# Performance work log

Measured on AMD Instinct MI355X. Metric: run time of the kernel, lower is better.

The kernel has to match this reference:

```python
import jax, jax.numpy as jnp
from jax import lax
import numpy as np

B = 4096        # num_batch
NVAR = 120      # 3 * num_legs(4) * horizon(10)
NC = 2 * NVAR   # num_constraints = 240
HID = 1024      # GRU hidden size
RIN = 3 * (NC + NVAR)  # GRU input dim = 1080
MAXITER = 8
RHO = 1.0
REG = 1e-4


def setup_inputs() -> dict:
    key = jax.random.key(0)
    ks = jax.random.split(key, 10)
    # SPD quadratic cost H, linear cost g, inequality constraints C x <= c
    M = jax.random.normal(ks[0], (NVAR, NVAR), jnp.float32)
    H = M @ M.T / NVAR + jnp.eye(NVAR, dtype=jnp.float32)
    g = jax.random.normal(ks[1], (NVAR,), jnp.float32)
    C = 0.1 * jax.random.normal(ks[2], (NC, NVAR), jnp.float32)
    c = jax.random.uniform(ks[3], (NC,), jnp.float32, 0.1, 1.0)
    lamda_init = jax.random.normal(ks[4], (B, NVAR), jnp.float32)
    s_init = jax.random.uniform(ks[5], (B, NC), jnp.float32)
    h_0 = jnp.zeros((B, HID), jnp.float32)
    # GRU cell (torch GRUCell layout: [3*HID, in]) + output head to NC+NVAR
    sc_i = 1.0 / np.sqrt(RIN)
    sc_h = 1.0 / np.sqrt(HID)
    W_ih = sc_i * jax.random.normal(ks[6], (3 * HID, RIN), jnp.float32)
    b_ih = jnp.zeros((3 * HID,), jnp.float32)
    W_hh = sc_h * jax.random.normal(ks[7], (3 * HID, HID), jnp.float32)
    b_hh = jnp.zeros((3 * HID,), jnp.float32)
    W_out = sc_h * jax.random.normal(ks[8], (NC + NVAR, HID), jnp.float32)
    b_out = jnp.zeros((NC + NVAR,), jnp.float32)
    return dict(lamda_init=lamda_init, s_init=s_init, h_0=h_0, H=H, g=g, C=C, c=c,
                W_ih=W_ih, b_ih=b_ih, W_hh=W_hh, b_hh=b_hh, W_out=W_out, b_out=b_out)


def _gru_cell(x, h, W_ih, b_ih, W_hh, b_hh):
    gi = x @ W_ih.T + b_ih
    gh = h @ W_hh.T + b_hh
    i_r, i_z, i_n = jnp.split(gi, 3, axis=1)
    h_r, h_z, h_n = jnp.split(gh, 3, axis=1)
    r = jax.nn.sigmoid(i_r + h_r)
    z = jax.nn.sigmoid(i_z + h_z)
    n = jnp.tanh(i_n + r * h_n)
    return (1.0 - z) * n + z * h


def reference(lamda_init, s_init, h_0, H, g, C, c, W_ih, b_ih, W_hh, b_hh, W_out, b_out):
    I = jnp.eye(NVAR, dtype=H.dtype)
    # ---- init solve (compute_projection_gru preamble) ----
    Q_inv0 = jnp.linalg.pinv(H + REG * I)
    lincost0 = -0.0 * lamda_init + g                 # [B, NVAR]
    xi0 = (-lincost0) @ Q_inv0.T                     # sol = (Qinv @ rhs.T).T
    s0 = jnp.maximum(0.0, -(xi0 @ C.T) + c)
    s0 = 0.0 * s_init + s0                           # s_init = 0*nn + 1*s_
    lam0 = lamda_init
    # ---- constant per-iteration projection matrix (same every iter) ----
    Q_inv = jnp.linalg.pinv(H + RHO * (C.T @ C) + REG * I)

    def step(carry, _):
        s, lam, h = carry
        # compute_feasible_control
        b_aug = c - s                                # [B, NC]
        lincost = -lam + g - RHO * (b_aug @ C)       # [B, NVAR]
        xi = (-lincost) @ Q_inv.T                    # [B, NVAR]
        Axi = xi @ C.T                               # [B, NC]
        s_new = jnp.maximum(0.0, -Axi + c)
        res_vec = Axi - c + s_new
        res_norm = jnp.linalg.norm(res_vec, axis=1)
        lam_new = lam - RHO * (res_vec @ C)
        qp_cost = 0.5 * (xi @ H @ xi.T) + xi @ g     # [B, B] (faithful to source)
        qp_norm = jnp.linalg.norm(qp_cost, axis=1)
        # GRU refinement
        r = jnp.concatenate([s, lam, s_new, lam_new, s_new - s, lam_new - lam], axis=1)
        h_new = _gru_cell(r, h, W_ih, b_ih, W_hh, b_hh)
        out = h_new @ W_out.T + b_out                # [B, NC+NVAR]
        s_fin = jnp.maximum(0.0, s_new + out[:, :NC])
        lam_fin = lam_new + out[:, NC:NC + NVAR]
        fixed = jnp.linalg.norm(lam - lam_fin, axis=1) + jnp.linalg.norm(s - s_fin, axis=1)
        return (s_fin, lam_fin, h_new), (xi, res_norm, fixed, qp_norm)

    (_, _, _), (xis, primal, fixed, qpres) = lax.scan(step, (s0, lam0, h_0), None, length=MAXITER)
    return xis[-1], primal, fixed, qpres
```

## Files before the change

kernel.cpp:

```cpp
#include <hip/hip_runtime.h>
#include <hip/hip_bf16.h>
#include <math.h>

#define NB    4096
#define NV    120
#define NCN   240
#define HIDD  1024
#define RINN  1080
#define NOUTD 360
#define NOUTP 384
#define NITER 8
#define REGEPS 1e-4f
#define NPART 256

#define KCAT 4224
#define HOFF 2176
#define KWC  2112
#define KWO  1024
#define NSTEP_R 34
#define NSTEPS  66

typedef unsigned short u16;
typedef __attribute__((ext_vector_type(8))) short short8v;
typedef __attribute__((ext_vector_type(4))) float f32x4;

__device__ inline u16 f2b(float x) {
    __hip_bfloat16 h = __float2bfloat16(x);
    return __builtin_bit_cast(u16, h);
}
__device__ inline float b2f(u16 u) {
    __hip_bfloat16 h = __builtin_bit_cast(__hip_bfloat16, u);
    return __bfloat162float(h);
}

__device__ inline void gl16(const void* g, void* l) {
    __builtin_amdgcn_global_load_lds(
        (__attribute__((address_space(1))) void*)(void*)g,
        (__attribute__((address_space(3))) void*)l, 16, 0, 0);
}

__global__ void k_buildA(const float* __restrict__ H, const float* __restrict__ C,
                         float* __restrict__ A, float* __restrict__ A0) {
    int i = blockIdx.x;
    int which = blockIdx.y;
    for (int j = threadIdx.x; j < NV; j += blockDim.x) {
        float v = H[i*NV + j] + (i == j ? REGEPS : 0.f);
        if (which == 0) {
            float acc = 0.f;
            for (int k = 0; k < NCN; ++k) acc += C[k*NV + i] * C[k*NV + j];
            A[i*NV + j] = v + acc;
        } else {
            A0[i*NV + j] = v;
        }
    }
}

__global__ void k_buildCT(const float* __restrict__ C, float* __restrict__ CT) {
    int j = blockIdx.x;
    for (int k = threadIdx.x; k < NCN; k += 256)
        CT[(size_t)j * NCN + k] = C[(size_t)k * NV + j];
}

__device__ inline void inv4x4(const float* m, float* inv) {
    float s0 = m[0]*m[5] - m[1]*m[4];
    float s1 = m[0]*m[6] - m[2]*m[4];
    float s2 = m[0]*m[7] - m[3]*m[4];
    float s3 = m[1]*m[6] - m[2]*m[5];
    float s4 = m[1]*m[7] - m[3]*m[5];
    float s5 = m[2]*m[7] - m[3]*m[6];
    float c5 = m[10]*m[15] - m[11]*m[14];
    float c4 = m[9]*m[15] - m[11]*m[13];
    float c3 = m[9]*m[14] - m[10]*m[13];
    float c2 = m[8]*m[15] - m[11]*m[12];
    float c1 = m[8]*m[14] - m[10]*m[12];
    float c0 = m[8]*m[13] - m[9]*m[12];
    float det = s0*c5 - s1*c4 + s2*c3 + s3*c2 - s4*c1 + s5*c0;
    float id = 1.0f / det;
    inv[0]  = ( m[5]*c5 - m[6]*c4 + m[7]*c3) * id;
    inv[1]  = (-m[1]*c5 + m[2]*c4 - m[3]*c3) * id;
    inv[2]  = ( m[13]*s5 - m[14]*s4 + m[15]*s3) * id;
    inv[3]  = (-m[9]*s5 + m[10]*s4 - m[11]*s3) * id;
    inv[4]  = (-m[4]*c5 + m[6]*c2 - m[7]*c1) * id;
    inv[5]  = ( m[0]*c5 - m[2]*c2 + m[3]*c1) * id;
    inv[6]  = (-m[12]*s5 + m[14]*s2 - m[15]*s1) * id;
    inv[7]  = ( m[8]*s5 - m[10]*s2 + m[11]*s1) * id;
    inv[8]  = ( m[4]*c4 - m[5]*c2 + m[7]*c0) * id;
    inv[9]  = (-m[0]*c4 + m[1]*c2 - m[3]*c0) * id;
    inv[10] = ( m[12]*s4 - m[13]*s2 + m[15]*s0) * id;
    inv[11] = (-m[8]*s4 + m[9]*s2 - m[11]*s0) * id;
    inv[12] = (-m[4]*c3 + m[5]*c1 - m[6]*c0) * id;
    inv[13] = ( m[0]*c3 - m[1]*c1 + m[2]*c0) * id;
    inv[14] = (-m[12]*s3 + m[13]*s1 - m[14]*s0) * id;
    inv[15] = ( m[8]*s3 - m[9]*s1 + m[10]*s0) * id;
}

__global__ __launch_bounds__(1024) void k_invert(const float* __restrict__ Ain,
                                                 const float* __restrict__ A0in,
                                                 float* __restrict__ Qi,
                                                 float* __restrict__ Qi0) {
    __shared__ float M[NV][132];
    __shared__ float Rl[4][132];
    __shared__ float Bl[16];
    const float* src = (blockIdx.x == 0) ? Ain : A0in;
    float* dst = (blockIdx.x == 0) ? Qi : Qi0;
    const int t = threadIdx.x;
    for (int idx = t; idx < NV*132; idx += 1024) {
        int i = idx / 132, j = idx - i*132;
        M[i][j] = (j < NV) ? src[i*NV + j] : 0.f;
    }
    __syncthreads();
    const int ty = t >> 5;
    const int g4 = (t & 31) * 4;
    for (int kk = 0; kk < NV; kk += 4) {
        if (ty == 0) {
            float a[16], b[16];
            #pragma unroll
            for (int p = 0; p < 4; ++p) {
                float4 v = *(const float4*)&M[kk + p][kk];
                a[p*4+0] = v.x; a[p*4+1] = v.y; a[p*4+2] = v.z; a[p*4+3] = v.w;
            }
            inv4x4(a, b);
            float4 m0v = *(const float4*)&M[kk+0][g4];
            float4 m1v = *(const float4*)&M[kk+1][g4];
            float4 m2v = *(const float4*)&M[kk+2][g4];
            float4 m3v = *(const float4*)&M[kk+3][g4];
            #pragma unroll
            for (int p = 0; p < 4; ++p) {
                float4 r;
                r.x = b[p*4+0]*m0v.x + b[p*4+1]*m1v.x + b[p*4+2]*m2v.x + b[p*4+3]*m3v.x;
                r.y = b[p*4+0]*m0v.y + b[p*4+1]*m1v.y + b[p*4+2]*m2v.y + b[p*4+3]*m3v.y;
                r.z = b[p*4+0]*m0v.z + b[p*4+1]*m1v.z + b[p*4+2]*m2v.z + b[p*4+3]*m3v.z;
                r.w = b[p*4+0]*m0v.w + b[p*4+1]*m1v.w + b[p*4+2]*m2v.w + b[p*4+3]*m3v.w;
                *(float4*)&Rl[p][g4] = r;
            }
            if (t < 16) Bl[t] = b[t];
        }
        float4 F[4];
        #pragma unroll
        for (int q = 0; q < 4; ++q) {
            int i = ty + 32*q;
            F[q] = (i < NV) ? *(const float4*)&M[i][kk] : float4{0.f,0.f,0.f,0.f};
        }
        __syncthreads();
        #pragma unroll
        for (int q = 0; q < 4; ++q) {
            int i = ty + 32*q;
            if (i < NV) {
                int dp = i - kk;
                bool ispiv = (dp >= 0) && (dp < 4);
                float4 v;
                if (g4 == kk) {
                    if (ispiv) {
                        v = *(const float4*)&Bl[dp*4];
                    } else {
                        v.x = -(F[q].x*Bl[0] + F[q].y*Bl[4] + F[q].z*Bl[8]  + F[q].w*Bl[12]);
                        v.y = -(F[q].x*Bl[1] + F[q].y*Bl[5] + F[q].z*Bl[9]  + F[q].w*Bl[13]);
                        v.z = -(F[q].x*Bl[2] + F[q].y*Bl[6] + F[q].z*Bl[10] + F[q].w*Bl[14]);
                        v.w = -(F[q].x*Bl[3] + F[q].y*Bl[7] + F[q].z*Bl[11] + F[q].w*Bl[15]);
                    }
                } else if (ispiv) {
                    v = *(const float4*)&Rl[dp][g4];
                } else {
                    float4 r0 = *(const float4*)&Rl[0][g4];
                    float4 r1 = *(const float4*)&Rl[1][g4];
                    float4 r2 = *(const float4*)&Rl[2][g4];
                    float4 r3 = *(const float4*)&Rl[3][g4];
                    v = *(const float4*)&M[i][g4];
                    v.x -= F[q].x*r0.x + F[q].y*r1.x + F[q].z*r2.x + F[q].w*r3.x;
                    v.y -= F[q].x*r0.y + F[q].y*r1.y + F[q].z*r2.y + F[q].w*r3.y;
                    v.z -= F[q].x*r0.z + F[q].y*r1.z + F[q].z*r2.z + F[q].w*r3.z;
                    v.w -= F[q].x*r0.w + F[q].y*r1.w + F[q].z*r2.w + F[q].w*r3.w;
                }
                *(float4*)&M[i][g4] = v;
            }
        }
        __syncthreads();
    }
    for (int idx = t; idx < NV*NV; idx += 1024) {
        int i = idx / NV, j = idx - i*NV;
        dst[idx] = M[i][j];
    }
}

__global__ void k_s0(const float* __restrict__ Qi0, const float* __restrict__ g,
                     const float* __restrict__ C, const float* __restrict__ c,
                     float* __restrict__ s0v) {
    __shared__ float xi0[NV];
    int t = threadIdx.x;
    if (t < NV) {
        float a = 0.f;
        for (int j = 0; j < NV; ++j) a += Qi0[t*NV + j] * g[j];
        xi0[t] = -a;
    }
    __syncthreads();
    if (t < NCN) {
        float a = 0.f;
        for (int j = 0; j < NV; ++j) a += C[t*NV + j] * xi0[j];
        s0v[t] = fmaxf(0.f, c[t] - a);
    }
}

__global__ void k_init(const float* __restrict__ s0v, const float* __restrict__ lam0,
                       float* __restrict__ s, float* __restrict__ lam) {
    int b0 = blockIdx.x * 8;
    int t = threadIdx.x;
    for (int idx = t; idx < 8*NCN; idx += 256) {
        int m = idx / NCN, k = idx % NCN;
        s[(size_t)(b0 + m)*NCN + k] = s0v[k];
    }
    for (int idx = t; idx < 8*NV; idx += 256) lam[(size_t)b0*NV + idx] = lam0[(size_t)b0*NV + idx];
}

__global__ void k_packH(const float* __restrict__ h0, u16* __restrict__ act) {
    int n = blockIdx.x;
    size_t base = (size_t)n * KCAT + HOFF;
    for (int k = threadIdx.x; k < HIDD; k += 256) {
        float x = h0[(size_t)n * HIDD + k];
        u16 hi = f2b(x);
        act[base + k] = hi;
        act[base + HIDD + k] = f2b(x - b2f(hi));
    }
}

__global__ void k_packWcat(const float* __restrict__ Wih, const float* __restrict__ Whh,
                           u16* __restrict__ Wc) {
    int n = blockIdx.x;
    size_t base = (size_t)n * KWC;
    for (int k = threadIdx.x; k < 1088; k += 256)
        Wc[base + k] = f2b(k < RINN ? Wih[(size_t)n * RINN + k] : 0.f);
    for (int k = threadIdx.x; k < HIDD; k += 256)
        Wc[base + 1088 + k] = f2b(Whh[(size_t)n * HIDD + k]);
}

__global__ void k_packWo(const float* __restrict__ src, u16* __restrict__ dst) {
    int n = blockIdx.x;
    size_t row = (size_t)n * KWO;
    for (int k = threadIdx.x; k < KWO; k += 256)
        dst[row + k] = f2b(n < NOUTD ? src[(size_t)n * HIDD + k] : 0.f);
}

__device__ inline void write2(u16* __restrict__ act, size_t base, int pos, float x) {
    u16 hi = f2b(x);
    u16 lo = f2b(x - b2f(hi));
    act[base + pos] = hi;
    act[base + 1088 + pos] = lo;
}

__device__ inline float hadd4(float4 v) { return (v.x + v.y) + (v.z + v.w); }

#define XB 8
__global__ __launch_bounds__(512) void k_xiproj(
        const float* __restrict__ s, const float* __restrict__ lam,
        const float* __restrict__ Cg, const float* __restrict__ CTg,
        const float* __restrict__ c,
        const float* __restrict__ g, const float* __restrict__ Qi,
        const float* __restrict__ Hg,
        float* __restrict__ xi, float* __restrict__ Y, float* __restrict__ wv,
        float* __restrict__ snew, float* __restrict__ lamn,
        u16* __restrict__ act, float* __restrict__ primal) {
    __shared__ float Msh[31680];
    __shared__ float bd[XB][NCN];
    __shared__ float ul[XB][NV];
    __shared__ float xl[XB][NV];
    __shared__ float resl[XB][NCN];
    const int b0 = blockIdx.x * XB;
    const int t = threadIdx.x;

    for (int idx = t; idx < XB*NCN; idx += 512) {
        int m = idx / NCN, k = idx - m*NCN;
        bd[m][k] = c[k] - s[(size_t)(b0 + m)*NCN + k];
    }
    for (int idx = t; idx < NV*NCN; idx += 512) {
        int i = idx / NCN, k = idx - i*NCN;
        Msh[i*244 + k] = CTg[idx];
    }
    __syncthreads();
    if (t < 240) {
        int m = t / 30, jb = t - (t / 30) * 30;
        float4 a0 = {0,0,0,0}, a1 = {0,0,0,0}, a2 = {0,0,0,0}, a3 = {0,0,0,0};
        for (int kg = 0; kg < 60; ++kg) {
            float4 b4 = *(const float4*)&bd[m][kg*4];
            float4 c0 = *(const float4*)&Msh[(jb     ) * 244 + kg*4];
            float4 c1 = *(const float4*)&Msh[(jb + 30) * 244 + kg*4];
            float4 c2 = *(const float4*)&Msh[(jb + 60) * 244 + kg*4];
            float4 c3 = *(const float4*)&Msh[(jb + 90) * 244 + kg*4];
            a0.x += b4.x*c0.x; a0.y += b4.y*c0.y; a0.z += b4.z*c0.z; a0.w += b4.w*c0.w;
            a1.x += b4.x*c1.x; a1.y += b4.y*c1.y; a1.z += b4.z*c1.z; a1.w += b4.w*c1.w;
            a2.x += b4.x*c2.x; a2.y += b4.y*c2.y; a2.z += b4.z*c2.z; a2.w += b4.w*c2.w;
            a3.x += b4.x*c3.x; a3.y += b4.y*c3.y; a3.z += b4.z*c3.z; a3.w += b4.w*c3.w;
        }
        #pragma unroll
        for (int p = 0; p < 4; ++p) {
            int j = jb + 30*p;
            float h = (p == 0) ? hadd4(a0) : (p == 1) ? hadd4(a1) : (p == 2) ? hadd4(a2) : hadd4(a3);
            ul[m][j] = lam[(size_t)(b0 + m)*NV + j] - g[j] + h;
        }
    }
    __syncthreads();
    for (int idx = t; idx < NV*NV; idx += 512) {
        int i = idx / NV, j = idx - i*NV;
        Msh[i*132 + j] = Qi[idx];
        Msh[(120 + i)*132 + j] = Hg[idx];
    }
    __syncthreads();
    if (t < 240) {
        int m = t / 30, ib = t - (t / 30) * 30;
        float4 a0 = {0,0,0,0}, a1 = {0,0,0,0}, a2 = {0,0,0,0}, a3 = {0,0,0,0};
        for (int jg = 0; jg < 30; ++jg) {
            float4 u4 = *(const float4*)&ul[m][jg*4];
            float4 q0 = *(const float4*)&Msh[(ib     ) * 132 + jg*4];
            float4 q1 = *(const float4*)&Msh[(ib + 30) * 132 + jg*4];
            float4 q2 = *(const float4*)&Msh[(ib + 60) * 132 + jg*4];
            float4 q3 = *(const float4*)&Msh[(ib + 90) * 132 + jg*4];
            a0.x += u4.x*q0.x; a0.y += u4.y*q0.y; a0.z += u4.z*q0.z; a0.w += u4.w*q0.w;
            a1.x += u4.x*q1.x; a1.y += u4.y*q1.y; a1.z += u4.z*q1.z; a1.w += u4.w*q1.w;
            a2.x += u4.x*q2.x; a2.y += u4.y*q2.y; a2.z += u4.z*q2.z; a2.w += u4.w*q2.w;
            a3.x += u4.x*q3.x; a3.y += u4.y*q3.y; a3.z += u4.z*q3.z; a3.w += u4.w*q3.w;
        }
        #pragma unroll
        for (int p = 0; p < 4; ++p) {
            int i = ib + 30*p;
            float a = (p == 0) ? hadd4(a0) : (p == 1) ? hadd4(a1) : (p == 2) ? hadd4(a2) : hadd4(a3);
            xl[m][i] = a;
            xi[(size_t)(b0 + m)*NV + i] = a;
        }
    }
    __syncthreads();
    if (t < 240) {
        int m = t / 30, ib = t - (t / 30) * 30;
        float4 a0 = {0,0,0,0}, a1 = {0,0,0,0}, a2 = {0,0,0,0}, a3 = {0,0,0,0};
        for (int jg = 0; jg < 30; ++jg) {
            float4 x4 = *(const float4*)&xl[m][jg*4];
            float4 h0 = *(const float4*)&Msh[(120 + ib     ) * 132 + jg*4];
            float4 h1 = *(const float4*)&Msh[(120 + ib + 30) * 132 + jg*4];
            float4 h2 = *(const float4*)&Msh[(120 + ib + 60) * 132 + jg*4];
            float4 h3 = *(const float4*)&Msh[(120 + ib + 90) * 132 + jg*4];
            a0.x += x4.x*h0.x; a0.y += x4.y*h0.y; a0.z += x4.z*h0.z; a0.w += x4.w*h0.w;
            a1.x += x4.x*h1.x; a1.y += x4.y*h1.y; a1.z += x4.z*h1.z; a1.w += x4.w*h1.w;
            a2.x += x4.x*h2.x; a2.y += x4.y*h2.y; a2.z += x4.z*h2.z; a2.w += x4.w*h2.w;
            a3.x += x4.x*h3.x; a3.y += x4.y*h3.y; a3.z += x4.z*h3.z; a3.w += x4.w*h3.w;
        }
        #pragma unroll
        for (int p = 0; p < 4; ++p) {
            int i = ib + 30*p;
            float a = (p == 0) ? hadd4(a0) : (p == 1) ? hadd4(a1) : (p == 2) ? hadd4(a2) : hadd4(a3);
            Y[(size_t)(b0 + m)*NV + i] = a;
        }
    }
    if (t >= 240 && t < 240 + XB) {
        int m = t - 240;
        float a = 0.f;
        for (int j = 0; j < NV; ++j) a += xl[m][j] * g[j];
        wv[b0 + m] = a;
    }
    __syncthreads();
    for (int idx = t; idx < NCN*NV; idx += 512) {
        int k = idx / NV, j = idx - k*NV;
        Msh[k*132 + j] = Cg[idx];
    }
    __syncthreads();
    if (t < 480) {
        int m = t / 60, kb = t - (t / 60) * 60;
        float4 a0 = {0,0,0,0}, a1 = {0,0,0,0}, a2 = {0,0,0,0}, a3 = {0,0,0,0};
        for (int jg = 0; jg < 30; ++jg) {
            float4 x4 = *(const float4*)&xl[m][jg*4];
            float4 c0 = *(const float4*)&Msh[(kb      ) * 132 + jg*4];
            float4 c1 = *(const float4*)&Msh[(kb + 60 ) * 132 + jg*4];
            float4 c2 = *(const float4*)&Msh[(kb + 120) * 132 + jg*4];
            float4 c3 = *(const float4*)&Msh[(kb + 180) * 132 + jg*4];
            a0.x += x4.x*c0.x; a0.y += x4.y*c0.y; a0.z += x4.z*c0.z; a0.w += x4.w*c0.w;
            a1.x += x4.x*c1.x; a1.y += x4.y*c1.y; a1.z += x4.z*c1.z; a1.w += x4.w*c1.w;
            a2.x += x4.x*c2.x; a2.y += x4.y*c2.y; a2.z += x4.z*c2.z; a2.w += x4.w*c2.w;
            a3.x += x4.x*c3.x; a3.y += x4.y*c3.y; a3.z += x4.z*c3.z; a3.w += x4.w*c3.w;
        }
        #pragma unroll
        for (int p = 0; p < 4; ++p) {
            int k = kb + 60*p;
            float a = (p == 0) ? hadd4(a0) : (p == 1) ? hadd4(a1) : (p == 2) ? hadd4(a2) : hadd4(a3);
            float sn = fmaxf(0.f, c[k] - a);
            float rv = a - c[k] + sn;
            resl[m][k] = rv;
            int b = b0 + m;
            snew[(size_t)b*NCN + k] = sn;
            float so = s[(size_t)b*NCN + k];
            size_t base = (size_t)b * KCAT;
            write2(act, base, k, so);
            write2(act, base, 360 + k, sn);
            write2(act, base, 720 + k, sn - so);
        }
    }
    __syncthreads();
    if (t < XB) {
        float a = 0.f;
        for (int k = 0; k < NCN; ++k) a += resl[t][k] * resl[t][k];
        primal[b0 + t] = sqrtf(a);
    }
    for (int idx = t; idx < NV*NCN; idx += 512) {
        int i = idx / NCN, k = idx - i*NCN;
        Msh[i*244 + k] = CTg[idx];
    }
    __syncthreads();
    if (t < 240) {
        int m = t / 30, ib = t - (t / 30) * 30;
        float4 a0 = {0,0,0,0}, a1 = {0,0,0,0}, a2 = {0,0,0,0}, a3 = {0,0,0,0};
        for (int kg = 0; kg < 60; ++kg) {
            float4 r4 = *(const float4*)&resl[m][kg*4];
            float4 c0 = *(const float4*)&Msh[(ib     ) * 244 + kg*4];
            float4 c1 = *(const float4*)&Msh[(ib + 30) * 244 + kg*4];
            float4 c2 = *(const float4*)&Msh[(ib + 60) * 244 + kg*4];
            float4 c3 = *(const float4*)&Msh[(ib + 90) * 244 + kg*4];
            a0.x += r4.x*c0.x; a0.y += r4.y*c0.y; a0.z += r4.z*c0.z; a0.w += r4.w*c0.w;
            a1.x += r4.x*c1.x; a1.y += r4.y*c1.y; a1.z += r4.z*c1.z; a1.w += r4.w*c1.w;
            a2.x += r4.x*c2.x; a2.y += r4.y*c2.y; a2.z += r4.z*c2.z; a2.w += r4.w*c2.w;
            a3.x += r4.x*c3.x; a3.y += r4.y*c3.y; a3.z += r4.z*c3.z; a3.w += r4.w*c3.w;
        }
        #pragma unroll
        for (int p = 0; p < 4; ++p) {
            int i = ib + 30*p;
            float a = (p == 0) ? hadd4(a0) : (p == 1) ? hadd4(a1) : (p == 2) ? hadd4(a2) : hadd4(a3);
            int b = b0 + m;
            float lo = lam[(size_t)b*NV + i];
            float ln = lo - a;
            lamn[(size_t)b*NV + i] = ln;
            size_t base = (size_t)b * KCAT;
            write2(act, base, 240 + i, lo);
            write2(act, base, 600 + i, ln);
            write2(act, base, 960 + i, ln - lo);
        }
    }
    for (int idx = t; idx < XB*8; idx += 512) {
        int m = idx >> 3, k = 1080 + (idx & 7);
        size_t base = (size_t)(b0 + m) * KCAT;
        act[base + k] = 0;
        act[base + 1088 + k] = 0;
    }
}

__global__ __launch_bounds__(256) void k_qp_part(const float* __restrict__ xi, const float* __restrict__ wv,
                         double* __restrict__ Gp, double* __restrict__ vp, double* __restrict__ Sp) {
    __shared__ float xl[16][NV];
    __shared__ float wl[16];
    int p = blockIdx.x;
    int b0 = p * 16;
    int t = threadIdx.x;
    for (int idx = t; idx < 16*NV; idx += 256) xl[idx/NV][idx%NV] = xi[(size_t)b0*NV + idx];
    if (t < 16) wl[t] = wv[b0 + t];
    __syncthreads();
    for (int idx = t; idx < NV*NV; idx += 256) {
        int i = idx / NV, j = idx % NV;
        double a = 0.0;
        for (int m = 0; m < 16; ++m) a += (double)xl[m][i] * (double)xl[m][j];
        Gp[(size_t)p*NV*NV + idx] = a;
    }
    if (t < NV) {
        double a = 0.0;
        for (int m = 0; m < 16; ++m) a += (double)wl[m] * (double)xl[m][t];
        vp[(size_t)p*NV + t] = a;
    }
    if (t == 0) {
        double a = 0.0;
        for (int m = 0; m < 16; ++m) a += (double)wl[m] * (double)wl[m];
        Sp[p] = a;
    }
}

__global__ void k_qp_red(const double* __restrict__ Gp, const double* __restrict__ vp,
                         const double* __restrict__ Sp,
                         double* __restrict__ G, double* __restrict__ v, double* __restrict__ S) {
    int idx = blockIdx.x * 256 + threadIdx.x;
    if (idx < NV*NV) {
        double a = 0.0;
        for (int p = 0; p < NPART; ++p) a += Gp[(size_t)p*NV*NV + idx];
        G[idx] = a;
    }
    if (idx < NV) {
        double a = 0.0;
        for (int p = 0; p < NPART; ++p) a += vp[(size_t)p*NV + idx];
        v[idx] = a;
    }
    if (idx == 0) {
        double a = 0.0;
        for (int p = 0; p < NPART; ++p) a += Sp[p];
        S[0] = a;
    }
}

__global__ __launch_bounds__(256) void k_qp_norm(const float* __restrict__ Y, const double* __restrict__ G,
                         const double* __restrict__ v, const double* __restrict__ S,
                         float* __restrict__ qp) {
    __shared__ float Yl[16][NV];
    __shared__ double tl[16][NV];
    int b0 = blockIdx.x * 16;
    int t = threadIdx.x;
    for (int idx = t; idx < 16*NV; idx += 256) Yl[idx/NV][idx%NV] = Y[(size_t)b0*NV + idx];
    __syncthreads();
    for (int idx = t; idx < 16*NV; idx += 256) {
        int m = idx / NV, i = idx % NV;
        double a = 0.0;
        for (int j = 0; j < NV; ++j) a += G[j*NV + i] * (double)Yl[m][j];
        tl[m][i] = a;
    }
    __syncthreads();
    if (t < 16) {
        double a = 0.0, bv = 0.0;
        for (int i = 0; i < NV; ++i) { a += (double)Yl[t][i] * tl[t][i]; bv += (double)Yl[t][i] * v[i]; }
        double q = 0.25 * a + bv + S[0];
        qp[b0 + t] = (float)sqrt(q > 0.0 ? q : 0.0);
    }
}

#define GRUF_STEP(NSLOT, BUFI) do {                                              \
    char* Ah_ = lds + (BUFI) * 32768;                                            \
    char* Al_ = Ah_ + 4096;                                                      \
    char* Bb_ = Ah_ + 8192;                                                      \
    const int srow = lane & 15;                                                  \
    const int ksl = lane >> 4;                                                   \
    short8v ah[2], al[2];                                                        \
    _Pragma("unroll")                                                            \
    for (int fm = 0; fm < 2; ++fm) {                                             \
        int rr = wm * 32 + fm * 16 + srow;                                       \
        int off = rr * 64 + ((ksl ^ ((rr >> 1) & 3)) << 4);                      \
        ah[fm] = *(const short8v*)(Ah_ + off);                                   \
        al[fm] = *(const short8v*)(Al_ + off);                                   \
    }                                                                            \
    _Pragma("unroll")                                                            \
    for (int fn = 0; fn < 2; ++fn) {                                             \
        int rb = wn * 32 + fn * 16 + srow;                                       \
        int boff = rb * 64 + ((ksl ^ ((rb >> 1) & 3)) << 4);                     \
        short8v bfr = *(const short8v*)(Bb_ + boff);                             \
        short8v bfz = *(const short8v*)(Bb_ + 8192 + boff);                      \
        short8v bfn = *(const short8v*)(Bb_ + 16384 + boff);                     \
        _Pragma("unroll")                                                        \
        for (int fm = 0; fm < 2; ++fm) {                                         \
            acc[0][fn][fm] = __builtin_amdgcn_mfma_f32_16x16x32_bf16(ah[fm], bfr, acc[0][fn][fm], 0, 0, 0); \
            acc[0][fn][fm] = __builtin_amdgcn_mfma_f32_16x16x32_bf16(al[fm], bfr, acc[0][fn][fm], 0, 0, 0); \
            acc[1][fn][fm] = __builtin_amdgcn_mfma_f32_16x16x32_bf16(ah[fm], bfz, acc[1][fn][fm], 0, 0, 0); \
            acc[1][fn][fm] = __builtin_amdgcn_mfma_f32_16x16x32_bf16(al[fm], bfz, acc[1][fn][fm], 0, 0, 0); \
            acc[NSLOT][fn][fm] = __builtin_amdgcn_mfma_f32_16x16x32_bf16(ah[fm], bfn, acc[NSLOT][fn][fm], 0, 0, 0); \
            acc[NSLOT][fn][fm] = __builtin_amdgcn_mfma_f32_16x16x32_bf16(al[fm], bfn, acc[NSLOT][fn][fm], 0, 0, 0); \
        }                                                                        \
    }                                                                            \
} while (0)

__global__ __launch_bounds__(512) void k_gruf(
        const u16* __restrict__ act,
        const u16* __restrict__ Wc,
        const float* __restrict__ bih, const float* __restrict__ bhh,
        u16* __restrict__ actn) {
    __shared__ char lds[65536];
    const int t = threadIdx.x;
    const int lane = t & 63;
    const int wid = t >> 6;
    const int wm = wid >> 2;
    const int wn = wid & 3;
    const int bid = blockIdx.x;
    const int xcd = bid & 7;
    const int slot = bid >> 3;
    const int m0 = (xcd * 8 + (slot & 7)) * 64;
    const int n0 = (slot >> 3) * 128;

    f32x4 acc[4][2][2];
    #pragma unroll
    for (int i = 0; i < 4; ++i)
        #pragma unroll
        for (int j = 0; j < 2; ++j)
            #pragma unroll
            for (int k = 0; k < 2; ++k) {
                f32x4 z = {0.f, 0.f, 0.f, 0.f};
                acc[i][j][k] = z;
            }

    auto stage = [&](int step, int buf) {
        char* Ah_ = lds + buf * 32768;
        char* Al_ = Ah_ + 4096;
        char* Bb_ = Ah_ + 8192;
        const int hiOff = (step < NSTEP_R) ? step * 32 : step * 32 + 1088;
        const int loOff = hiOff + ((step < NSTEP_R) ? 1088 : 1024);
        const int wOff = step * 32;
        {
            int rr = (wid & 3) * 16 + (lane >> 2);
            int kq = ((lane & 3) ^ ((rr >> 1) & 3)) << 3;
            if (wid < 4)
                gl16(act + (size_t)(m0 + rr) * KCAT + hiOff + kq, Ah_ + (wid & 3) * 1024);
            else
                gl16(act + (size_t)(m0 + rr) * KCAT + loOff + kq, Al_ + (wid & 3) * 1024);
        }
        #pragma unroll
        for (int j = 0; j < 3; ++j) {
            int cb = wid * 3 + j;
            int rbg = cb * 16 + (lane >> 2);
            int kq = ((lane & 3) ^ ((rbg >> 1) & 3)) << 3;
            gl16(Wc + (size_t)((rbg >> 7) * 1024 + n0 + (rbg & 127)) * KWC + wOff + kq,
                 Bb_ + cb * 1024);
        }
    };

    stage(0, 0);
    __syncthreads();
    int cur = 0;
    for (int step = 0; step < NSTEP_R; ++step) {
        stage(step + 1, cur ^ 1);
        GRUF_STEP(2, cur);
        __syncthreads();
        cur ^= 1;
    }
    for (int step = NSTEP_R; step < NSTEPS; ++step) {
        if (step + 1 < NSTEPS) stage(step + 1, cur ^ 1);
        GRUF_STEP(3, cur);
        __syncthreads();
        cur ^= 1;
    }

    #pragma unroll
    for (int fn = 0; fn < 2; ++fn) {
        const int jj = n0 + wn * 32 + fn * 16 + (lane & 15);
        const float bir = bih[jj],        bhr = bhh[jj];
        const float biz = bih[1024 + jj], bhz = bhh[1024 + jj];
        const float bin = bih[2048 + jj], bhn = bhh[2048 + jj];
        #pragma unroll
        for (int fm = 0; fm < 2; ++fm) {
            #pragma unroll
            for (int rg = 0; rg < 4; ++rg) {
                int m = m0 + wm * 32 + fm * 16 + (lane >> 4) * 4 + rg;
                float rz = acc[0][fn][fm][rg];
                float zz = acc[1][fn][fm][rg];
                float inn = acc[2][fn][fm][rg];
                float hnn = acc[3][fn][fm][rg];
                float rgate = 1.f / (1.f + expf(-(rz + bir + bhr)));
                float zgate = 1.f / (1.f + expf(-(zz + biz + bhz)));
                float ngate = tanhf(inn + bin + rgate * (hnn + bhn));
                size_t base = (size_t)m * KCAT + HOFF;
                float hv = b2f(act[base + jj]) + b2f(act[base + HIDD + jj]);
                float hnew = (1.f - zgate) * ngate + zgate * hv;
                u16 nh = f2b(hnew);
                actn[base + jj] = nh;
                actn[base + HIDD + jj] = f2b(hnew - b2f(nh));
            }
        }
    }
}

__global__ __launch_bounds__(512) void k_outp(
        const u16* __restrict__ act, const u16* __restrict__ Wo,
        const float* __restrict__ bo, float* __restrict__ outb) {
    __shared__ char lds[32768];
    const int t = threadIdx.x;
    const int lane = t & 63;
    const int wid = t >> 6;
    const int wm = wid >> 2;
    const int wn = wid & 3;
    const int m0 = blockIdx.x * 64;
    const int n0 = blockIdx.y * 128;
    f32x4 acc[2][2];
    #pragma unroll
    for (int i = 0; i < 2; ++i)
        #pragma unroll
        for (int j = 0; j < 2; ++j) {
            f32x4 z = {0.f, 0.f, 0.f, 0.f};
            acc[i][j] = z;
        }

    auto stage = [&](int step, int buf) {
        char* Ah_ = lds + buf * 16384;
        char* Al_ = Ah_ + 4096;
        char* Bb_ = Ah_ + 8192;
        {
            int rr = (wid & 3) * 16 + (lane >> 2);
            int kq = ((lane & 3) ^ ((rr >> 1) & 3)) << 3;
            if (wid < 4)
                gl16(act + (size_t)(m0 + rr) * KCAT + HOFF + step * 32 + kq,
                     Ah_ + (wid & 3) * 1024);
            else
                gl16(act + (size_t)(m0 + rr) * KCAT + HOFF + HIDD + step * 32 + kq,
                     Al_ + (wid & 3) * 1024);
        }
        {
            int rb = wid * 16 + (lane >> 2);
            int kq = ((lane & 3) ^ ((rb >> 1) & 3)) << 3;
            gl16(Wo + (size_t)(n0 + rb) * KWO + step * 32 + kq, Bb_ + wid * 1024);
        }
    };

    stage(0, 0);
    __syncthreads();
    int cur = 0;
    for (int step = 0; step < 32; ++step) {
        if (step + 1 < 32) stage(step + 1, cur ^ 1);
        {
            char* Ah_ = lds + cur * 16384;
            char* Al_ = Ah_ + 4096;
            char* Bb_ = Ah_ + 8192;
            const int srow = lane & 15;
            const int ksl = lane >> 4;
            short8v ah[2], al[2];
            #pragma unroll
            for (int fm = 0; fm < 2; ++fm) {
                int rr = wm * 32 + fm * 16 + srow;
                int off = rr * 64 + ((ksl ^ ((rr >> 1) & 3)) << 4);
                ah[fm] = *(const short8v*)(Ah_ + off);
                al[fm] = *(const short8v*)(Al_ + off);
            }
            #pragma unroll
            for (int fn = 0; fn < 2; ++fn) {
                int rb = wn * 32 + fn * 16 + srow;
                int boff = rb * 64 + ((ksl ^ ((rb >> 1) & 3)) << 4);
                short8v bf = *(const short8v*)(Bb_ + boff);
                #pragma unroll
                for (int fm = 0; fm < 2; ++fm) {
                    acc[fn][fm] = __builtin_amdgcn_mfma_f32_16x16x32_bf16(ah[fm], bf, acc[fn][fm], 0, 0, 0);
                    acc[fn][fm] = __builtin_amdgcn_mfma_f32_16x16x32_bf16(al[fm], bf, acc[fn][fm], 0, 0, 0);
                }
            }
        }
        __syncthreads();
        cur ^= 1;
    }
    #pragma unroll
    for (int fn = 0; fn < 2; ++fn) {
        int n = n0 + wn * 32 + fn * 16 + (lane & 15);
        if (n < NOUTD) {
            float bb = bo[n];
            #pragma unroll
            for (int fm = 0; fm < 2; ++fm) {
                #pragma unroll
                for (int rg = 0; rg < 4; ++rg) {
                    int m = m0 + wm * 32 + fm * 16 + (lane >> 4) * 4 + rg;
                    outb[(size_t)m * NOUTP + n] = acc[fn][fm][rg] + bb;
                }
            }
        }
    }
}

__global__ __launch_bounds__(256) void k_fin(const float* __restrict__ snew, const float* __restrict__ lamn,
                     const float* __restrict__ outb,
                     float* __restrict__ s, float* __restrict__ lam,
                     float* __restrict__ fx) {
    __shared__ float redS[16][17];
    __shared__ float redL[16][17];
    int b0 = blockIdx.x * 16;
    int tm = threadIdx.x / 16;
    int tk = threadIdx.x % 16;
    int b = b0 + tm;
    float ds2 = 0.f, dl2 = 0.f;
    for (int k = tk; k < NCN; k += 16) {
        float o = outb[(size_t)b*NOUTP + k];
        float sf = fmaxf(0.f, snew[(size_t)b*NCN + k] + o);
        float so = s[(size_t)b*NCN + k];
        s[(size_t)b*NCN + k] = sf;
        float d = so - sf;
        ds2 += d * d;
    }
    for (int i = tk; i < NV; i += 16) {
        float o = outb[(size_t)b*NOUTP + NCN + i];
        float lf = lamn[(size_t)b*NV + i] + o;
        float lo = lam[(size_t)b*NV + i];
        lam[(size_t)b*NV + i] = lf;
        float d = lo - lf;
        dl2 += d * d;
    }
    redS[tm][tk] = ds2;
    redL[tm][tk] = dl2;
    __syncthreads();
    if (tk == 0) {
        float a = 0.f, l = 0.f;
        for (int q = 0; q < 16; ++q) { a += redS[tm][q]; l += redL[tm][q]; }
        fx[b] = sqrtf(l) + sqrtf(a);
    }
}

extern "C" void kernel_launch(void* const* d_in, const int* in_sizes, int n_in,
                              void* d_out, int out_size, void* d_ws, size_t ws_size,
                              hipStream_t stream) {
    const float* lamda_init = (const float*)d_in[0];
    const float* h0    = (const float*)d_in[2];
    const float* H     = (const float*)d_in[3];
    const float* g     = (const float*)d_in[4];
    const float* C     = (const float*)d_in[5];
    const float* c     = (const float*)d_in[6];
    const float* W_ih  = (const float*)d_in[7];
    const float* b_ih  = (const float*)d_in[8];
    const float* W_hh  = (const float*)d_in[9];
    const float* b_hh  = (const float*)d_in[10];
    const float* W_out = (const float*)d_in[11];
    const float* b_out = (const float*)d_in[12];

    float* out    = (float*)d_out;
    float* xi_out = out;
    float* primal = out + (size_t)NB*NV;
    float* fixedo = primal + (size_t)NITER*NB;
    float* qpres  = fixedo + (size_t)NITER*NB;

    char* wp = (char*)d_ws;
    auto alloc = [&](size_t bytes) {
        void* p = (void*)wp;
        wp += (bytes + 255) & ~(size_t)255;
        return p;
    };
    float* Amat  = (float*)alloc(NV*NV*4);
    float* A0m   = (float*)alloc(NV*NV*4);
    float* Qinv  = (float*)alloc(NV*NV*4);
    float* Qinv0 = (float*)alloc(NV*NV*4);
    float* CTg   = (float*)alloc((size_t)NV*NCN*4);
    float* s0v   = (float*)alloc(NCN*4);
    float* sbuf  = (float*)alloc((size_t)NB*NCN*4);
    float* snew  = (float*)alloc((size_t)NB*NCN*4);
    float* lam   = (float*)alloc((size_t)NB*NV*4);
    float* lamn  = (float*)alloc((size_t)NB*NV*4);
    float* xib   = (float*)alloc((size_t)NB*NV*4);
    float* Yb    = (float*)alloc((size_t)NB*NV*4);
    float* wb    = (float*)alloc(NB*4);
    float* outb  = (float*)alloc((size_t)NB*NOUTP*4);
    u16* actA    = (u16*)alloc((size_t)NB*KCAT*2);
    u16* actB    = (u16*)alloc((size_t)NB*KCAT*2);
    u16* Wcat    = (u16*)alloc((size_t)3072*KWC*2);
    u16* Wopk    = (u16*)alloc((size_t)NOUTP*KWO*2);
    double* Gpart = (double*)alloc((size_t)NPART*NV*NV*8);
    double* vpart = (double*)alloc((size_t)NPART*NV*8);
    double* Spart = (double*)alloc(NPART*8);
    double* Gfin  = (double*)alloc(NV*NV*8);
    double* vfin  = (double*)alloc(NV*8);
    double* Sfin  = (double*)alloc(8);

    k_buildA<<<dim3(NV, 2), dim3(128), 0, stream>>>(H, C, Amat, A0m);
    k_buildCT<<<dim3(NV), dim3(256), 0, stream>>>(C, CTg);
    k_invert<<<dim3(2), dim3(1024), 0, stream>>>(Amat, A0m, Qinv, Qinv0);
    k_s0<<<dim3(1), dim3(256), 0, stream>>>(Qinv0, g, C, c, s0v);
    k_init<<<dim3(NB/8), dim3(256), 0, stream>>>(s0v, lamda_init, sbuf, lam);
    k_packWcat<<<dim3(3072), dim3(256), 0, stream>>>(W_ih, W_hh, Wcat);
    k_packWo<<<dim3(NOUTP), dim3(256), 0, stream>>>(W_out, Wopk);
    k_packH<<<dim3(NB), dim3(256), 0, stream>>>(h0, actA);

    u16* hc = actA;
    u16* hn2 = actB;
    for (int it = 0; it < NITER; ++it) {
        k_xiproj<<<dim3(NB/XB), dim3(512), 0, stream>>>(sbuf, lam, C, CTg, c, g, Qinv, H,
                                                        xib, Yb, wb, snew, lamn, hc,
                                                        primal + (size_t)it*NB);
        k_qp_part<<<dim3(NPART), dim3(256), 0, stream>>>(xib, wb, Gpart, vpart, Spart);
        k_qp_red<<<dim3((NV*NV + 255)/256), dim3(256), 0, stream>>>(Gpart, vpart, Spart, Gfin, vfin, Sfin);
        k_qp_norm<<<dim3(NB/16), dim3(256), 0, stream>>>(Yb, Gfin, vfin, Sfin, qpres + (size_t)it*NB);
        k_gruf<<<dim3(512), dim3(512), 0, stream>>>(hc, Wcat, b_ih, b_hh, hn2);
        k_outp<<<dim3(64, 3), dim3(512), 0, stream>>>(hn2, Wopk, b_out, outb);
        k_fin<<<dim3(NB/16), dim3(256), 0, stream>>>(snew, lamn, outb, sbuf, lam, fixedo + (size_t)it*NB);
        u16* tmp = hc; hc = hn2; hn2 = tmp;
    }
    hipMemcpyAsync(xi_out, xib, (size_t)NB*NV*sizeof(float), hipMemcpyDeviceToDevice, stream);
}
```

Before: 2.195 ms.

## Drop bf16 low-part MFMAs in GRU GEMMs and fuse QP and finalize kernels

The GRU gate and output GEMMs no longer stage or multiply the low bf16 residual of the split activations, so only the high part is used. This halves the MFMA count and the activation loads, at the cost of numerical accuracy. Separately, the QP partial Gram sums are folded into k_xiproj with 512 partitions of 8 rows, and k_qp_norm is merged with k_fin into one tail kernel. Together these cut kernel launches and the intermediate wv buffer.

```diff
diff --git a/kernel.cpp b/kernel.cpp
--- a/kernel.cpp
+++ b/kernel.cpp
@@ -11,7 +11,7 @@
 #define NOUTP 384
 #define NITER 8
 #define REGEPS 1e-4f
-#define NPART 256
+#define NPART 512
 
 #define KCAT 4224
 #define HOFF 2176
@@ -255,14 +255,16 @@
         const float* __restrict__ c,
         const float* __restrict__ g, const float* __restrict__ Qi,
         const float* __restrict__ Hg,
-        float* __restrict__ xi, float* __restrict__ Y, float* __restrict__ wv,
+        float* __restrict__ xi, float* __restrict__ Y,
         float* __restrict__ snew, float* __restrict__ lamn,
-        u16* __restrict__ act, float* __restrict__ primal) {
+        u16* __restrict__ act, float* __restrict__ primal,
+        double* __restrict__ Gp, double* __restrict__ vp, double* __restrict__ Sp) {
     __shared__ float Msh[31680];
     __shared__ float bd[XB][NCN];
     __shared__ float ul[XB][NV];
     __shared__ float xl[XB][NV];
     __shared__ float resl[XB][NCN];
+    __shared__ float wl[XB];
     const int b0 = blockIdx.x * XB;
     const int t = threadIdx.x;
 
@@ -351,7 +353,7 @@
         int m = t - 240;
         float a = 0.f;
         for (int j = 0; j < NV; ++j) a += xl[m][j] * g[j];
-        wv[b0 + m] = a;
+        wl[m] = a;
     }
     __syncthreads();
     for (int idx = t; idx < NCN*NV; idx += 512) {
@@ -434,33 +436,24 @@
         act[base + k] = 0;
         act[base + 1088 + k] = 0;
     }
-}
-
-__global__ __launch_bounds__(256) void k_qp_part(const float* __restrict__ xi, const float* __restrict__ wv,
-                         double* __restrict__ Gp, double* __restrict__ vp, double* __restrict__ Sp) {
-    __shared__ float xl[16][NV];
-    __shared__ float wl[16];
-    int p = blockIdx.x;
-    int b0 = p * 16;
-    int t = threadIdx.x;
-    for (int idx = t; idx < 16*NV; idx += 256) xl[idx/NV][idx%NV] = xi[(size_t)b0*NV + idx];
-    if (t < 16) wl[t] = wv[b0 + t];
-    __syncthreads();
-    for (int idx = t; idx < NV*NV; idx += 256) {
-        int i = idx / NV, j = idx % NV;
+    for (int idx = t; idx < NV*NV; idx += 512) {
+        int i = idx / NV, j = idx - i*NV;
         double a = 0.0;
-        for (int m = 0; m < 16; ++m) a += (double)xl[m][i] * (double)xl[m][j];
-        Gp[(size_t)p*NV*NV + idx] = a;
+        #pragma unroll
+        for (int m = 0; m < XB; ++m) a += (double)xl[m][i] * (double)xl[m][j];
+        Gp[(size_t)blockIdx.x*NV*NV + idx] = a;
     }
     if (t < NV) {
         double a = 0.0;
-        for (int m = 0; m < 16; ++m) a += (double)wl[m] * (double)xl[m][t];
-        vp[(size_t)p*NV + t] = a;
+        #pragma unroll
+        for (int m = 0; m < XB; ++m) a += (double)wl[m] * (double)xl[m][t];
+        vp[(size_t)blockIdx.x*NV + t] = a;
     }
     if (t == 0) {
         double a = 0.0;
-        for (int m = 0; m < 16; ++m) a += (double)wl[m] * (double)wl[m];
-        Sp[p] = a;
+        #pragma unroll
+        for (int m = 0; m < XB; ++m) a += (double)wl[m] * (double)wl[m];
+        Sp[blockIdx.x] = a;
     }
 }
 
@@ -485,14 +478,21 @@
     }
 }
 
-__global__ __launch_bounds__(256) void k_qp_norm(const float* __restrict__ Y, const double* __restrict__ G,
-                         const double* __restrict__ v, const double* __restrict__ S,
-                         float* __restrict__ qp) {
+__global__ __launch_bounds__(256) void k_tail(
+        const float* __restrict__ Yb, const double* __restrict__ G,
+        const double* __restrict__ v, const double* __restrict__ S,
+        float* __restrict__ qp,
+        const float* __restrict__ snew, const float* __restrict__ lamn,
+        const float* __restrict__ outb,
+        float* __restrict__ s, float* __restrict__ lam,
+        float* __restrict__ fx) {
     __shared__ float Yl[16][NV];
     __shared__ double tl[16][NV];
+    __shared__ float redS[16][17];
+    __shared__ float redL[16][17];
     int b0 = blockIdx.x * 16;
     int t = threadIdx.x;
-    for (int idx = t; idx < 16*NV; idx += 256) Yl[idx/NV][idx%NV] = Y[(size_t)b0*NV + idx];
+    for (int idx = t; idx < 16*NV; idx += 256) Yl[idx/NV][idx%NV] = Yb[(size_t)b0*NV + idx];
     __syncthreads();
     for (int idx = t; idx < 16*NV; idx += 256) {
         int m = idx / NV, i = idx % NV;
@@ -507,21 +507,47 @@
         double q = 0.25 * a + bv + S[0];
         qp[b0 + t] = (float)sqrt(q > 0.0 ? q : 0.0);
     }
+    int tm = t / 16;
+    int tk = t % 16;
+    int b = b0 + tm;
+    float ds2 = 0.f, dl2 = 0.f;
+    for (int k = tk; k < NCN; k += 16) {
+        float o = outb[(size_t)b*NOUTP + k];
+        float sf = fmaxf(0.f, snew[(size_t)b*NCN + k] + o);
+        float so = s[(size_t)b*NCN + k];
+        s[(size_t)b*NCN + k] = sf;
+        float d = so - sf;
+        ds2 += d * d;
+    }
+    for (int i = tk; i < NV; i += 16) {
+        float o = outb[(size_t)b*NOUTP + NCN + i];
+        float lf = lamn[(size_t)b*NV + i] + o;
+        float lo = lam[(size_t)b*NV + i];
+        lam[(size_t)b*NV + i] = lf;
+        float d = lo - lf;
+        dl2 += d * d;
+    }
+    redS[tm][tk] = ds2;
+    redL[tm][tk] = dl2;
+    __syncthreads();
+    if (tk == 0) {
+        float a = 0.f, l = 0.f;
+        for (int q = 0; q < 16; ++q) { a += redS[tm][q]; l += redL[tm][q]; }
+        fx[b] = sqrtf(l) + sqrtf(a);
+    }
 }
 
 #define GRUF_STEP(NSLOT, BUFI) do {                                              \
     char* Ah_ = lds + (BUFI) * 32768;                                            \
-    char* Al_ = Ah_ + 4096;                                                      \
     char* Bb_ = Ah_ + 8192;                                                      \
     const int srow = lane & 15;                                                  \
     const int ksl = lane >> 4;                                                   \
-    short8v ah[2], al[2];                                                        \
+    short8v ah[2];                                                               \
     _Pragma("unroll")                                                            \
     for (int fm = 0; fm < 2; ++fm) {                                             \
         int rr = wm * 32 + fm * 16 + srow;                                       \
         int off = rr * 64 + ((ksl ^ ((rr >> 1) & 3)) << 4);                      \
         ah[fm] = *(const short8v*)(Ah_ + off);                                   \
-        al[fm] = *(const short8v*)(Al_ + off);                                   \
     }                                                                            \
     _Pragma("unroll")                                                            \
     for (int fn = 0; fn < 2; ++fn) {                                             \
@@ -533,11 +559,8 @@
         _Pragma("unroll")                                                        \
         for (int fm = 0; fm < 2; ++fm) {                                         \
             acc[0][fn][fm] = __builtin_amdgcn_mfma_f32_16x16x32_bf16(ah[fm], bfr, acc[0][fn][fm], 0, 0, 0); \
-            acc[0][fn][fm] = __builtin_amdgcn_mfma_f32_16x16x32_bf16(al[fm], bfr, acc[0][fn][fm], 0, 0, 0); \
             acc[1][fn][fm] = __builtin_amdgcn_mfma_f32_16x16x32_bf16(ah[fm], bfz, acc[1][fn][fm], 0, 0, 0); \
-            acc[1][fn][fm] = __builtin_amdgcn_mfma_f32_16x16x32_bf16(al[fm], bfz, acc[1][fn][fm], 0, 0, 0); \
             acc[NSLOT][fn][fm] = __builtin_amdgcn_mfma_f32_16x16x32_bf16(ah[fm], bfn, acc[NSLOT][fn][fm], 0, 0, 0); \
-            acc[NSLOT][fn][fm] = __builtin_amdgcn_mfma_f32_16x16x32_bf16(al[fm], bfn, acc[NSLOT][fn][fm], 0, 0, 0); \
         }                                                                        \
     }                                                                            \
 } while (0)
@@ -572,18 +595,13 @@
 
     auto stage = [&](int step, int buf) {
         char* Ah_ = lds + buf * 32768;
-        char* Al_ = Ah_ + 4096;
         char* Bb_ = Ah_ + 8192;
         const int hiOff = (step < NSTEP_R) ? step * 32 : step * 32 + 1088;
-        const int loOff = hiOff + ((step < NSTEP_R) ? 1088 : 1024);
         const int wOff = step * 32;
-        {
+        if (wid < 4) {
             int rr = (wid & 3) * 16 + (lane >> 2);
             int kq = ((lane & 3) ^ ((rr >> 1) & 3)) << 3;
-            if (wid < 4)
-                gl16(act + (size_t)(m0 + rr) * KCAT + hiOff + kq, Ah_ + (wid & 3) * 1024);
-            else
-                gl16(act + (size_t)(m0 + rr) * KCAT + loOff + kq, Al_ + (wid & 3) * 1024);
+            gl16(act + (size_t)(m0 + rr) * KCAT + hiOff + kq, Ah_ + (wid & 3) * 1024);
         }
         #pragma unroll
         for (int j = 0; j < 3; ++j) {
@@ -662,17 +680,12 @@
 
     auto stage = [&](int step, int buf) {
         char* Ah_ = lds + buf * 16384;
-        char* Al_ = Ah_ + 4096;
         char* Bb_ = Ah_ + 8192;
-        {
+        if (wid < 4) {
             int rr = (wid & 3) * 16 + (lane >> 2);
             int kq = ((lane & 3) ^ ((rr >> 1) & 3)) << 3;
-            if (wid < 4)
-                gl16(act + (size_t)(m0 + rr) * KCAT + HOFF + step * 32 + kq,
-                     Ah_ + (wid & 3) * 1024);
-            else
-                gl16(act + (size_t)(m0 + rr) * KCAT + HOFF + HIDD + step * 32 + kq,
-                     Al_ + (wid & 3) * 1024);
+            gl16(act + (size_t)(m0 + rr) * KCAT + HOFF + step * 32 + kq,
+                 Ah_ + (wid & 3) * 1024);
         }
         {
             int rb = wid * 16 + (lane >> 2);
@@ -688,17 +701,15 @@
         if (step + 1 < 32) stage(step + 1, cur ^ 1);
         {
             char* Ah_ = lds + cur * 16384;
-            char* Al_ = Ah_ + 4096;
             char* Bb_ = Ah_ + 8192;
             const int srow = lane & 15;
             const int ksl = lane >> 4;
-            short8v ah[2], al[2];
+            short8v ah[2];
             #pragma unroll
             for (int fm = 0; fm < 2; ++fm) {
                 int rr = wm * 32 + fm * 16 + srow;
                 int off = rr * 64 + ((ksl ^ ((rr >> 1) & 3)) << 4);
                 ah[fm] = *(const short8v*)(Ah_ + off);
-                al[fm] = *(const short8v*)(Al_ + off);
             }
             #pragma unroll
             for (int fn = 0; fn < 2; ++fn) {
@@ -706,10 +717,8 @@
                 int boff = rb * 64 + ((ksl ^ ((rb >> 1) & 3)) << 4);
                 short8v bf = *(const short8v*)(Bb_ + boff);
                 #pragma unroll
-                for (int fm = 0; fm < 2; ++fm) {
+                for (int fm = 0; fm < 2; ++fm)
                     acc[fn][fm] = __builtin_amdgcn_mfma_f32_16x16x32_bf16(ah[fm], bf, acc[fn][fm], 0, 0, 0);
-                    acc[fn][fm] = __builtin_amdgcn_mfma_f32_16x16x32_bf16(al[fm], bf, acc[fn][fm], 0, 0, 0);
-                }
             }
         }
         __syncthreads();
@@ -729,43 +738,6 @@
                 }
             }
         }
-    }
-}
-
-__global__ __launch_bounds__(256) void k_fin(const float* __restrict__ snew, const float* __restrict__ lamn,
-                     const float* __restrict__ outb,
-                     float* __restrict__ s, float* __restrict__ lam,
-                     float* __restrict__ fx) {
-    __shared__ float redS[16][17];
-    __shared__ float redL[16][17];
-    int b0 = blockIdx.x * 16;
-    int tm = threadIdx.x / 16;
-    int tk = threadIdx.x % 16;
-    int b = b0 + tm;
-    float ds2 = 0.f, dl2 = 0.f;
-    for (int k = tk; k < NCN; k += 16) {
-        float o = outb[(size_t)b*NOUTP + k];
-        float sf = fmaxf(0.f, snew[(size_t)b*NCN + k] + o);
-        float so = s[(size_t)b*NCN + k];
-        s[(size_t)b*NCN + k] = sf;
-        float d = so - sf;
-        ds2 += d * d;
-    }
-    for (int i = tk; i < NV; i += 16) {
-        float o = outb[(size_t)b*NOUTP + NCN + i];
-        float lf = lamn[(size_t)b*NV + i] + o;
-        float lo = lam[(size_t)b*NV + i];
-        lam[(size_t)b*NV + i] = lf;
-        float d = lo - lf;
-        dl2 += d * d;
-    }
-    redS[tm][tk] = ds2;
-    redL[tm][tk] = dl2;
-    __syncthreads();
-    if (tk == 0) {
-        float a = 0.f, l = 0.f;
-        for (int q = 0; q < 16; ++q) { a += redS[tm][q]; l += redL[tm][q]; }
-        fx[b] = sqrtf(l) + sqrtf(a);
     }
 }
 
@@ -809,7 +781,6 @@
     float* lamn  = (float*)alloc((size_t)NB*NV*4);
     float* xib   = (float*)alloc((size_t)NB*NV*4);
     float* Yb    = (float*)alloc((size_t)NB*NV*4);
-    float* wb    = (float*)alloc(NB*4);
     float* outb  = (float*)alloc((size_t)NB*NOUTP*4);
     u16* actA    = (u16*)alloc((size_t)NB*KCAT*2);
     u16* actB    = (u16*)alloc((size_t)NB*KCAT*2);
@@ -835,14 +806,16 @@
     u16* hn2 = actB;
     for (int it = 0; it < NITER; ++it) {
         k_xiproj<<<dim3(NB/XB), dim3(512), 0, stream>>>(sbuf, lam, C, CTg, c, g, Qinv, H,
-                                                        xib, Yb, wb, snew, lamn, hc,
-                                                        primal + (size_t)it*NB);
-        k_qp_part<<<dim3(NPART), dim3(256), 0, stream>>>(xib, wb, Gpart, vpart, Spart);
+                                                        xib, Yb, snew, lamn, hc,
+                                                        primal + (size_t)it*NB,
+                                                        Gpart, vpart, Spart);
         k_qp_red<<<dim3((NV*NV + 255)/256), dim3(256), 0, stream>>>(Gpart, vpart, Spart, Gfin, vfin, Sfin);
-        k_qp_norm<<<dim3(NB/16), dim3(256), 0, stream>>>(Yb, Gfin, vfin, Sfin, qpres + (size_t)it*NB);
         k_gruf<<<dim3(512), dim3(512), 0, stream>>>(hc, Wcat, b_ih, b_hh, hn2);
         k_outp<<<dim3(64, 3), dim3(512), 0, stream>>>(hn2, Wopk, b_out, outb);
-        k_fin<<<dim3(NB/16), dim3(256), 0, stream>>>(snew, lamn, outb, sbuf, lam, fixedo + (size_t)it*NB);
+        k_tail<<<dim3(NB/16), dim3(256), 0, stream>>>(Yb, Gfin, vfin, Sfin,
+                                                      qpres + (size_t)it*NB,
+                                                      snew, lamn, outb, sbuf, lam,
+                                                      fixedo + (size_t)it*NB);
         u16* tmp = hc; hc = hn2; hn2 = tmp;
     }
     hipMemcpyAsync(xi_out, xib, (size_t)NB*NV*sizeof(float), hipMemcpyDeviceToDevice, stream);
```

Result: slower. 2.395 ms (+9.1%).
